# Performance work log

Hardware: AMD Instinct MI355X
Metric: run time of the kernel (lower is better)

## Reference

```python
import jax, jax.numpy as jnp
import numpy as np

INPUT_SZ, HIDDEN_SZ, OUTPUT_SZ, NUM_LAYERS, EMBED_SZ = 128, 512, 64, 4, 16
SEQ_LEN, BATCH = 128, 256


def setup_inputs() -> dict:
    key = jax.random.key(0)
    ks = jax.random.split(key, 12)
    H, E, L = HIDDEN_SZ, EMBED_SZ, NUM_LAYERS
    s = 0.05
    inp = {
        "input": jax.random.randint(ks[0], (SEQ_LEN, BATCH), 0, INPUT_SZ),
        "embed": jax.random.normal(ks[1], (INPUT_SZ, E), jnp.float32) * s,
        # layer 0 (input dim = E), dims: [dir=2, 4H, in]
        "Wih0": jax.random.normal(ks[2], (2, 4 * H, E), jnp.float32) * s,
        "Whh0": jax.random.normal(ks[3], (2, 4 * H, H), jnp.float32) * s,
        "bih0": jax.random.normal(ks[4], (2, 4 * H), jnp.float32) * s,
        "bhh0": jax.random.normal(ks[5], (2, 4 * H), jnp.float32) * s,
        # layers 1..L-1 (input dim = 2H)
        "Wih": jax.random.normal(ks[6], (L - 1, 2, 4 * H, 2 * H), jnp.float32) * s,
        "Whh": jax.random.normal(ks[7], (L - 1, 2, 4 * H, H), jnp.float32) * s,
        "bih": jax.random.normal(ks[8], (L - 1, 2, 4 * H), jnp.float32) * s,
        "bhh": jax.random.normal(ks[9], (L - 1, 2, 4 * H), jnp.float32) * s,
        "fc_w": jax.random.normal(ks[10], (OUTPUT_SZ, 4 * L * H), jnp.float32) * s,
        "fc_b": jax.random.normal(ks[11], (OUTPUT_SZ,), jnp.float32) * s,
    }
    return inp


def _lstm_forward(tokens, embed, Wih0, Whh0, bih0, bhh0, Wih, Whh, bih, bhh, fc_w, fc_b):
    L, H = NUM_LAYERS, HIDDEN_SZ
    T, B = tokens.shape
    xs = embed[tokens]  # [T, B, E]

    def step(carry, x_t):
        h, c = carry  # each [L, 2, B, H]
        x = x_t       # [B, in_dim]
        new_h, new_c = [], []
        for l in range(L):
            Wi = Wih0 if l == 0 else Wih[l - 1]
            Wh = Whh0 if l == 0 else Whh[l - 1]
            b = (bih0 + bhh0) if l == 0 else (bih[l - 1] + bhh[l - 1])
            # both directions see the same single-timestep input (PyTorch
            # bidirectional LSTM called with seq_len=1 per step)
            gates = (jnp.einsum('bi,dgi->dbg', x, Wi)
                     + jnp.einsum('dbh,dgh->dbg', h[l], Wh)
                     + b[:, None, :])  # [2, B, 4H]
            i_g, f_g, g_g, o_g = jnp.split(gates, 4, axis=-1)
            c_new = jax.nn.sigmoid(f_g) * c[l] + jax.nn.sigmoid(i_g) * jnp.tanh(g_g)
            h_new = jax.nn.sigmoid(o_g) * jnp.tanh(c_new)  # [2, B, H]
            new_h.append(h_new)
            new_c.append(c_new)
            x = jnp.concatenate([h_new[0], h_new[1]], axis=-1)  # [B, 2H]
        return (jnp.stack(new_h), jnp.stack(new_c)), None

    h0 = jnp.zeros((L, 2, B, H), xs.dtype)
    c0 = jnp.zeros((L, 2, B, H), xs.dtype)
    (h, c), _ = jax.lax.scan(step, (h0, c0), xs)

    # PyTorch layout: [2L, B, H], layer-major / direction-minor
    h = h.reshape(2 * L, B, H)
    c = c.reshape(2 * L, B, H)
    hid = jnp.concatenate([h, c], axis=2)                 # [2L, B, 2H]
    hid = hid.transpose(1, 0, 2).reshape(B, 4 * L * H)    # cat over 2L slices on dim 1
    out = hid @ fc_w.T + fc_b
    # dropout is identity at inference
    return jax.nn.softmax(out, axis=1)


def reference(input, embed, Wih0, Whh0, bih0, bhh0, Wih, Whh, bih, bhh, fc_w, fc_b):
    return _lstm_forward(input, embed, Wih0, Whh0, bih0, bhh0, Wih, Whh, bih, bhh, fc_w, fc_b)
```

## Files before the change

kernel.cpp:

```cpp
#include <hip/hip_runtime.h>

using short8 = __attribute__((ext_vector_type(8))) short;
using f32x4  = __attribute__((ext_vector_type(4))) float;
using f32x2  = __attribute__((ext_vector_type(2))) float;

static constexpr size_t N_WF0 = (size_t)2*32*8*3*4*512;
static constexpr size_t N_WF1 = (size_t)6*32*8*6*4*512;
static constexpr size_t N_WF  = N_WF0 + N_WF1;
static constexpr size_t N_BSE = (size_t)8*2048;
static constexpr size_t N_XPE = (size_t)128*2*256*8;
static constexpr size_t N_HBE = (size_t)2*8*64*256*8;
static constexpr size_t N_CBE = (size_t)8*256*512;
static constexpr size_t N_FCT = (size_t)8192*64;
static constexpr size_t N_FL  = (size_t)8*128;

static constexpr size_t OFF_WF = 0;
static constexpr size_t OFF_BS = OFF_WF + N_WF*2;
static constexpr size_t OFF_XP = OFF_BS + N_BSE*4;
static constexpr size_t OFF_HB = OFF_XP + N_XPE*2;
static constexpr size_t OFF_CB = OFF_HB + N_HBE*2;
static constexpr size_t OFF_HF = OFF_CB + N_CBE*4;
static constexpr size_t OFF_FC = OFF_HF + N_CBE*4;
static constexpr size_t OFF_FL = OFF_FC + N_FCT*4;
static constexpr size_t WS_NEEDED = OFF_FL + N_FL*4;

__device__ __forceinline__ short f2bf(float f) {
  unsigned u = __float_as_uint(f);
  u += 0x7fff + ((u >> 16) & 1);
  return (short)(u >> 16);
}

__device__ __forceinline__ void wait_ge(int* f, int target) {
  while (__hip_atomic_load(f, __ATOMIC_RELAXED, __HIP_MEMORY_SCOPE_AGENT) < target)
    __builtin_amdgcn_s_sleep(2);
}

__global__ void k_prep_wf(const float* __restrict__ Wih0, const float* __restrict__ Whh0,
                          const float* __restrict__ Wih,  const float* __restrict__ Whh,
                          short* __restrict__ Wf) {
  size_t idx = (size_t)blockIdx.x * blockDim.x + threadIdx.x;
  if (idx >= N_WF) return;
  int j  = (int)(idx & 7);
  int lane = (int)((idx >> 3) & 63);
  int gt = (int)((idx >> 9) & 3);
  int lr = lane & 15, qq = lane >> 4;
  float v;
  if (idx < N_WF0) {
    size_t rest = idx >> 11;
    int sl = (int)(rest % 3); size_t r2 = rest / 3;
    int wvv = (int)(r2 & 7);  size_t r3 = r2 >> 3;
    int ncc = (int)(r3 & 31); int dd = (int)(r3 >> 5);
    int g = gt*512 + ncc*16 + lr;
    int k = (wvv*3 + sl)*32 + qq*8 + j;
    if (k < 16)       v = Wih0[((size_t)dd*2048 + g)*16 + k];
    else if (k < 64)  v = 0.f;
    else if (k < 576) v = Whh0[((size_t)dd*2048 + g)*512 + (k - 64)];
    else              v = 0.f;
  } else {
    size_t u = idx - N_WF0;
    size_t rest = u >> 11;
    int sl = (int)(rest % 6); size_t r2 = rest / 6;
    int wvv = (int)(r2 & 7);  size_t r3 = r2 >> 3;
    int ncc = (int)(r3 & 31); int ldm = (int)(r3 >> 5);
    int g = gt*512 + ncc*16 + lr;
    int k = (wvv*6 + sl)*32 + qq*8 + j;
    if (k < 1024) v = Wih[((size_t)ldm*2048 + g)*1024 + k];
    else          v = Whh[((size_t)ldm*2048 + g)*512 + (k - 1024)];
  }
  Wf[idx] = f2bf(v);
}

__global__ void k_prep_bias(const float* __restrict__ bih0, const float* __restrict__ bhh0,
                            const float* __restrict__ bih, const float* __restrict__ bhh,
                            float* __restrict__ bsum) {
  int idx = blockIdx.x * blockDim.x + threadIdx.x;
  if (idx >= (int)N_BSE) return;
  int g = idx & 2047;
  int dd = (idx >> 11) & 1;
  int ll = idx >> 12;
  float v;
  if (ll == 0) v = bih0[dd*2048 + g] + bhh0[dd*2048 + g];
  else         v = bih[((ll-1)*2 + dd)*2048 + g] + bhh[((ll-1)*2 + dd)*2048 + g];
  bsum[idx] = v;
}

__global__ void k_prep_xp(const int* __restrict__ tok, const float* __restrict__ embed,
                          short* __restrict__ XP) {
  int idx = blockIdx.x * blockDim.x + threadIdx.x;
  if (idx >= (int)N_XPE) return;
  int i  = idx & 7;
  int b  = (idx >> 3) & 255;
  int kg = (idx >> 11) & 1;
  int t  = idx >> 12;
  int k = kg*8 + i;
  XP[idx] = f2bf(embed[tok[t*256 + b]*16 + k]);
}

__global__ void k_prep_fcT(const float* __restrict__ fc_w, float* __restrict__ fcT) {
  int idx = blockIdx.x * blockDim.x + threadIdx.x;
  if (idx >= (int)N_FCT) return;
  int o = idx & 63;
  int k = idx >> 6;
  fcT[idx] = fc_w[o * 8192 + k];
}

__global__ void __launch_bounds__(512, 2)
k_lstm(const short* __restrict__ Wf, const float* __restrict__ bsum,
       const short* __restrict__ XP, short* __restrict__ hb,
       float* __restrict__ cb, float* __restrict__ hf, int* __restrict__ Fl) {
  const int blk = blockIdx.x;
  const int ld = blk & 7, nc = blk >> 3;
  const int l = ld >> 1, d = ld & 1;
  const int tid = threadIdx.x;
  const int wv = tid >> 6, lane = tid & 63;
  const int q = lane >> 4, lr = lane & 15;
  const int SLb = (l == 0) ? 3 : 6;
  const size_t HB_LD = 131072;

  __shared__ float red[2][8][4][16][16];

  const int eu  = tid >> 7;
  const int en  = (tid >> 3) & 15;
  const int emh = tid & 7;
  float bias4[4];
  if (tid < 256) {
    #pragma unroll
    for (int gt = 0; gt < 4; ++gt)
      bias4[gt] = bsum[ld*2048 + gt*512 + nc*16 + en];
  }

  short8 wreg[6][4];
  {
    const short* wb = (l == 0)
      ? (Wf + (size_t)(d*32 + nc) * (8*3*4*512) + (size_t)wv * (3*4*512))
      : (Wf + N_WF0 + (size_t)((ld - 2)*32 + nc) * (8*6*4*512) + (size_t)wv * (6*4*512));
    #pragma unroll
    for (int sl = 0; sl < 6; ++sl) {
      #pragma unroll
      for (int gt = 0; gt < 4; ++gt) {
        if (sl < SLb) wreg[sl][gt] = *(const short8*)(wb + (sl*4 + gt)*512 + lane*8);
        else          wreg[sl][gt] = short8{0,0,0,0,0,0,0,0};
      }
    }
  }

  float* cbl = cb + (size_t)ld * (256*512);

  for (int t = 0; t < 128; ++t) {
    if (tid == 0) {
      if (t > 0) wait_ge(Fl + ld*128 + (t-1), 32);
      if (l > 0) {
        wait_ge(Fl + (ld-2-d)*128 + t, 32);
        wait_ge(Fl + (ld-1-d)*128 + t, 32);
      }
      if (l < 3 && t >= 2) {
        wait_ge(Fl + (2*l+2)*128 + (t-2), 32);
        wait_ge(Fl + (2*l+3)*128 + (t-2), 32);
      }
    }
    __syncthreads();
    __builtin_amdgcn_fence(__ATOMIC_ACQUIRE, "agent");

    const int pt = t & 1, pm = pt ^ 1;
    const short* apl[6];
    #pragma unroll
    for (int sl = 0; sl < 6; ++sl) {
      int S = wv * SLb + sl;
      const short* p; int lo;
      if (l == 0) {
        if (S < 2) { p = XP + (size_t)t * 4096; lo = (q < 1 ? q : 1) * 2048 + lr * 8; }
        else {
          int klb = (S <= 17) ? (4*S - 8) : 0;
          p = hb + (size_t)(pm*8 + ld) * HB_LD + (size_t)klb * 2048;
          lo = q * 2048 + lr * 8;
        }
      } else {
        const int pl0 = ld - 2 - d;
        if (S < 16)      p = hb + (size_t)(pt*8 + pl0    ) * HB_LD + (size_t)(4*S      ) * 2048;
        else if (S < 32) p = hb + (size_t)(pt*8 + pl0 + 1) * HB_LD + (size_t)(4*S - 64 ) * 2048;
        else             p = hb + (size_t)(pm*8 + ld     ) * HB_LD + (size_t)(4*S - 128) * 2048;
        lo = q * 2048 + lr * 8;
      }
      apl[sl] = p + lo;
    }

    short8 a[6][2];
    #pragma unroll
    for (int sl = 0; sl < 6; ++sl)
      if (sl < SLb) {
        a[sl][0] = *(const short8*)(apl[sl]);
        a[sl][1] = *(const short8*)(apl[sl] + 128);
      }

    for (int ro = 0; ro < 8; ++ro) {
      float c0 = 0.f, c1 = 0.f; int b0 = 0, b1 = 0, ej = 0;
      if (tid < 256) {
        ej = nc*16 + en;
        b0 = (ro*2 + eu)*16 + emh*2;
        b1 = b0 + 1;
        c0 = cbl[(size_t)b0*512 + ej];
        c1 = cbl[(size_t)b1*512 + ej];
      }
      f32x4 acc[2][4];
      #pragma unroll
      for (int u = 0; u < 2; ++u)
        #pragma unroll
        for (int gt = 0; gt < 4; ++gt) acc[u][gt] = f32x4{0.f,0.f,0.f,0.f};
      #pragma unroll
      for (int sl = 0; sl < 6; ++sl)
        if (sl < SLb) {
          #pragma unroll
          for (int gt = 0; gt < 4; ++gt) {
            acc[0][gt] = __builtin_amdgcn_mfma_f32_16x16x32_bf16(a[sl][0], wreg[sl][gt], acc[0][gt], 0,0,0);
            acc[1][gt] = __builtin_amdgcn_mfma_f32_16x16x32_bf16(a[sl][1], wreg[sl][gt], acc[1][gt], 0,0,0);
          }
        }
      if (ro < 7) {
        const int mo = (ro + 1) * 256;
        #pragma unroll
        for (int sl = 0; sl < 6; ++sl)
          if (sl < SLb) {
            a[sl][0] = *(const short8*)(apl[sl] + mo);
            a[sl][1] = *(const short8*)(apl[sl] + mo + 128);
          }
      }
      #pragma unroll
      for (int u = 0; u < 2; ++u)
        #pragma unroll
        for (int gt = 0; gt < 4; ++gt)
          *(f32x4*)&red[u][wv][gt][lr][q*4] = acc[u][gt];
      __syncthreads();
      if (tid < 256) {
        float g2[4][2];
        #pragma unroll
        for (int gt = 0; gt < 4; ++gt) {
          f32x2 sum = f32x2{0.f, 0.f};
          #pragma unroll
          for (int w8 = 0; w8 < 8; ++w8)
            sum += *(const f32x2*)&red[eu][w8][gt][en][emh*2];
          g2[gt][0] = sum[0] + bias4[gt];
          g2[gt][1] = sum[1] + bias4[gt];
        }
        short* hw = hb + (size_t)(pt*8 + ld) * HB_LD;
        #pragma unroll
        for (int e = 0; e < 2; ++e) {
          float gi = g2[0][e], gf = g2[1][e], gg = g2[2][e], go = g2[3][e];
          float si = 1.f/(1.f + __expf(-gi));
          float sf = 1.f/(1.f + __expf(-gf));
          float so = 1.f/(1.f + __expf(-go));
          float tg = 1.f - 2.f/(1.f + __expf(2.f*gg));
          float cold = e ? c1 : c0;
          int   b    = e ? b1 : b0;
          float cn = sf * cold + si * tg;
          float tc = 1.f - 2.f/(1.f + __expf(2.f*cn));
          float hn = so * tc;
          cbl[(size_t)b*512 + ej] = cn;
          hw[((size_t)(ej >> 3) * 256 + b) * 8 + (ej & 7)] = f2bf(hn);
          if (t == 127) hf[((size_t)ld*256 + b)*512 + ej] = hn;
        }
      }
      __syncthreads();
    }

    if (tid == 0)
      __hip_atomic_fetch_add(Fl + ld*128 + t, 1, __ATOMIC_RELEASE, __HIP_MEMORY_SCOPE_AGENT);
  }
}

__global__ void __launch_bounds__(256)
k_fc(const float* __restrict__ hf, const float* __restrict__ cb,
     const float* __restrict__ fcT, const float* __restrict__ fc_b,
     float* __restrict__ out) {
  const int tid = threadIdx.x;
  const int o = tid & 63;
  const int qw = tid >> 6;
  const int bi = blockIdx.x * 4 + qw;
  __shared__ float hidc[4][128];
  float acc = 0.f;
  for (int k0 = 0; k0 < 8192; k0 += 128) {
    #pragma unroll
    for (int c = 0; c < 2; ++c) {
      int idx = tid + c * 256;
      int r = idx >> 7, kk = idx & 127;
      int k = k0 + kk;
      int sS = k >> 10, rem = k & 1023, part = rem >> 9, j = rem & 511;
      const float* src = part ? cb : hf;
      hidc[r][kk] = src[((size_t)sS * 256 + (blockIdx.x * 4 + r)) * 512 + j];
    }
    __syncthreads();
    const float* hrow = hidc[qw];
    #pragma unroll 8
    for (int kk = 0; kk < 128; ++kk)
      acc += hrow[kk] * fcT[(size_t)(k0 + kk) * 64 + o];
    __syncthreads();
  }
  float v = acc + fc_b[o];
  float m = v;
  #pragma unroll
  for (int off = 32; off; off >>= 1) m = fmaxf(m, __shfl_xor(m, off, 64));
  float e = __expf(v - m);
  float ssum = e;
  #pragma unroll
  for (int off = 32; off; off >>= 1) ssum += __shfl_xor(ssum, off, 64);
  out[bi * 64 + o] = e / ssum;
}

extern "C" void kernel_launch(void* const* d_in, const int* in_sizes, int n_in,
                              void* d_out, int out_size, void* d_ws, size_t ws_size,
                              hipStream_t stream) {
  const int*   tok   = (const int*)d_in[0];
  const float* embed = (const float*)d_in[1];
  const float* Wih0  = (const float*)d_in[2];
  const float* Whh0  = (const float*)d_in[3];
  const float* bih0  = (const float*)d_in[4];
  const float* bhh0  = (const float*)d_in[5];
  const float* Wih   = (const float*)d_in[6];
  const float* Whh   = (const float*)d_in[7];
  const float* bih   = (const float*)d_in[8];
  const float* bhh   = (const float*)d_in[9];
  const float* fc_w  = (const float*)d_in[10];
  const float* fc_b  = (const float*)d_in[11];
  float* out = (float*)d_out;

  if (ws_size < WS_NEEDED) return;

  char* ws = (char*)d_ws;
  short* Wfb  = (short*)(ws + OFF_WF);
  float* bsum = (float*)(ws + OFF_BS);
  short* XP   = (short*)(ws + OFF_XP);
  short* hbuf = (short*)(ws + OFF_HB);
  float* cbuf = (float*)(ws + OFF_CB);
  float* hfb  = (float*)(ws + OFF_HF);
  float* fcT  = (float*)(ws + OFF_FC);
  int*   flg  = (int*)  (ws + OFF_FL);

  hipMemsetAsync(ws + OFF_HB + N_HBE, 0, N_HBE, stream);
  hipMemsetAsync(ws + OFF_CB, 0, N_CBE * 4, stream);
  hipMemsetAsync(ws + OFF_FL, 0, N_FL * 4, stream);

  k_prep_wf  <<<(int)((N_WF  + 255) / 256), 256, 0, stream>>>(Wih0, Whh0, Wih, Whh, Wfb);
  k_prep_bias<<<(int)((N_BSE + 255) / 256), 256, 0, stream>>>(bih0, bhh0, bih, bhh, bsum);
  k_prep_xp  <<<(int)((N_XPE + 255) / 256), 256, 0, stream>>>(tok, embed, XP);
  k_prep_fcT <<<(int)((N_FCT + 255) / 256), 256, 0, stream>>>(fc_w, fcT);

  void* kargs[] = {(void*)&Wfb, (void*)&bsum, (void*)&XP,
                   (void*)&hbuf, (void*)&cbuf, (void*)&hfb, (void*)&flg};
  hipLaunchCooperativeKernel((void*)k_lstm, dim3(256), dim3(512), kargs, 0, stream);

  k_fc<<<64, 256, 0, stream>>>(hfb, cbuf, fcT, fc_b, out);
}
```

Measured before the change: 6.139 ms.

## Stream LSTM activations into LDS via async global_load_lds double buffering, keep cell state in LDS

```diff
diff --git a/kernel.cpp b/kernel.cpp
--- a/kernel.cpp
+++ b/kernel.cpp
@@ -2,7 +2,6 @@
 
 using short8 = __attribute__((ext_vector_type(8))) short;
 using f32x4  = __attribute__((ext_vector_type(4))) float;
-using f32x2  = __attribute__((ext_vector_type(2))) float;
 
 static constexpr size_t N_WF0 = (size_t)2*32*8*3*4*512;
 static constexpr size_t N_WF1 = (size_t)6*32*8*6*4*512;
@@ -24,6 +23,11 @@
 static constexpr size_t OFF_FL = OFF_FC + N_FCT*4;
 static constexpr size_t WS_NEEDED = OFF_FL + N_FL*4;
 
+static constexpr int LDS_A   = 2*8*6*1024;
+static constexpr int LDS_RED = 8*4*16*20*4;
+static constexpr int LDS_C   = 16*256*4;
+static constexpr int LDS_TOT = LDS_A + LDS_RED + LDS_C;
+
 __device__ __forceinline__ short f2bf(float f) {
   unsigned u = __float_as_uint(f);
   u += 0x7fff + ((u >> 16) & 1);
@@ -32,7 +36,19 @@
 
 __device__ __forceinline__ void wait_ge(int* f, int target) {
   while (__hip_atomic_load(f, __ATOMIC_RELAXED, __HIP_MEMORY_SCOPE_AGENT) < target)
-    __builtin_amdgcn_s_sleep(2);
+    __builtin_amdgcn_s_sleep(1);
+}
+
+__device__ __forceinline__ void dma16(const void* g, void* l) {
+  __builtin_amdgcn_global_load_lds((const __attribute__((address_space(1))) unsigned int*)g,
+                                   (__attribute__((address_space(3))) unsigned int*)l, 16, 0, 0);
+}
+
+__device__ __forceinline__ void lds_barrier() {
+  __builtin_amdgcn_sched_barrier(0);
+  __builtin_amdgcn_s_waitcnt(0xC07F);
+  __builtin_amdgcn_s_barrier();
+  __builtin_amdgcn_sched_barrier(0);
 }
 
 __global__ void k_prep_wf(const float* __restrict__ Wih0, const float* __restrict__ Whh0,
@@ -107,26 +123,32 @@
 __global__ void __launch_bounds__(512, 2)
 k_lstm(const short* __restrict__ Wf, const float* __restrict__ bsum,
        const short* __restrict__ XP, short* __restrict__ hb,
-       float* __restrict__ cb, float* __restrict__ hf, int* __restrict__ Fl) {
+       float* __restrict__ cF, float* __restrict__ hf, int* __restrict__ Fl) {
+  extern __shared__ char smem[];
+  char*  As  = smem;
+  float* red = (float*)(smem + LDS_A);
+  float* cL  = (float*)(smem + LDS_A + LDS_RED);
+
   const int blk = blockIdx.x;
   const int ld = blk & 7, nc = blk >> 3;
   const int l = ld >> 1, d = ld & 1;
   const int tid = threadIdx.x;
   const int wv = tid >> 6, lane = tid & 63;
   const int q = lane >> 4, lr = lane & 15;
-  const int SLb = (l == 0) ? 3 : 6;
+  const int li = lane & 15, lk = lane >> 4;
+  const int SL = (l == 0) ? 3 : 6;
+  const int SUMW = (l == 0) ? 6 : 8;
+  const bool act = (l > 0) || (wv < 6);
   const size_t HB_LD = 131072;
 
-  __shared__ float red[2][8][4][16][16];
-
-  const int eu  = tid >> 7;
-  const int en  = (tid >> 3) & 15;
-  const int emh = tid & 7;
-  float bias4[4];
+  for (int i = tid; i < 4096; i += 512) cL[i] = 0.f;
+
+  float b4[4];
   if (tid < 256) {
+    int en = tid & 15;
     #pragma unroll
     for (int gt = 0; gt < 4; ++gt)
-      bias4[gt] = bsum[ld*2048 + gt*512 + nc*16 + en];
+      b4[gt] = bsum[ld*2048 + gt*512 + nc*16 + en];
   }
 
   short8 wreg[6][4];
@@ -138,128 +160,113 @@
     for (int sl = 0; sl < 6; ++sl) {
       #pragma unroll
       for (int gt = 0; gt < 4; ++gt) {
-        if (sl < SLb) wreg[sl][gt] = *(const short8*)(wb + (sl*4 + gt)*512 + lane*8);
-        else          wreg[sl][gt] = short8{0,0,0,0,0,0,0,0};
-      }
-    }
-  }
-
-  float* cbl = cb + (size_t)ld * (256*512);
+        if (sl < SL) wreg[sl][gt] = *(const short8*)(wb + (sl*4 + gt)*512 + lane*8);
+        else         wreg[sl][gt] = short8{0,0,0,0,0,0,0,0};
+      }
+    }
+  }
+  __syncthreads();
 
   for (int t = 0; t < 128; ++t) {
-    if (tid == 0) {
-      if (t > 0) wait_ge(Fl + ld*128 + (t-1), 32);
-      if (l > 0) {
-        wait_ge(Fl + (ld-2-d)*128 + t, 32);
-        wait_ge(Fl + (ld-1-d)*128 + t, 32);
-      }
-      if (l < 3 && t >= 2) {
-        wait_ge(Fl + (2*l+2)*128 + (t-2), 32);
-        wait_ge(Fl + (2*l+3)*128 + (t-2), 32);
-      }
-    }
+    if (tid == 0 && t > 0)           wait_ge(Fl + ld*128 + (t-1), 32);
+    if (tid == 1 && l > 0)           wait_ge(Fl + (ld-2-d)*128 + t, 32);
+    if (tid == 2 && l > 0)           wait_ge(Fl + (ld-1-d)*128 + t, 32);
+    if (tid == 3 && l < 3 && t >= 2) wait_ge(Fl + (2*l+2)*128 + (t-2), 32);
+    if (tid == 4 && l < 3 && t >= 2) wait_ge(Fl + (2*l+3)*128 + (t-2), 32);
     __syncthreads();
     __builtin_amdgcn_fence(__ATOMIC_ACQUIRE, "agent");
 
     const int pt = t & 1, pm = pt ^ 1;
+
     const short* apl[6];
     #pragma unroll
     for (int sl = 0; sl < 6; ++sl) {
-      int S = wv * SLb + sl;
-      const short* p; int lo;
-      if (l == 0) {
-        if (S < 2) { p = XP + (size_t)t * 4096; lo = (q < 1 ? q : 1) * 2048 + lr * 8; }
-        else {
-          int klb = (S <= 17) ? (4*S - 8) : 0;
-          p = hb + (size_t)(pm*8 + ld) * HB_LD + (size_t)klb * 2048;
-          lo = q * 2048 + lr * 8;
+      if (sl < SL && act) {
+        int S = wv * SL + sl;
+        const short* p;
+        if (l == 0) {
+          if (S < 2) p = XP + (size_t)t*4096 + (size_t)(lk & 1)*2048;
+          else       p = hb + (size_t)(pm*8 + ld)*HB_LD + (size_t)(4*S - 8 + lk)*2048;
+        } else {
+          const int pl0 = ld - 2 - d;
+          if (S < 16)      p = hb + (size_t)(pt*8 + pl0    )*HB_LD + (size_t)(4*S       + lk)*2048;
+          else if (S < 32) p = hb + (size_t)(pt*8 + pl0 + 1)*HB_LD + (size_t)(4*S - 64  + lk)*2048;
+          else             p = hb + (size_t)(pm*8 + ld     )*HB_LD + (size_t)(4*S - 128 + lk)*2048;
         }
-      } else {
-        const int pl0 = ld - 2 - d;
-        if (S < 16)      p = hb + (size_t)(pt*8 + pl0    ) * HB_LD + (size_t)(4*S      ) * 2048;
-        else if (S < 32) p = hb + (size_t)(pt*8 + pl0 + 1) * HB_LD + (size_t)(4*S - 64 ) * 2048;
-        else             p = hb + (size_t)(pm*8 + ld     ) * HB_LD + (size_t)(4*S - 128) * 2048;
-        lo = q * 2048 + lr * 8;
-      }
-      apl[sl] = p + lo;
-    }
-
-    short8 a[6][2];
-    #pragma unroll
-    for (int sl = 0; sl < 6; ++sl)
-      if (sl < SLb) {
-        a[sl][0] = *(const short8*)(apl[sl]);
-        a[sl][1] = *(const short8*)(apl[sl] + 128);
-      }
-
-    for (int ro = 0; ro < 8; ++ro) {
-      float c0 = 0.f, c1 = 0.f; int b0 = 0, b1 = 0, ej = 0;
-      if (tid < 256) {
-        ej = nc*16 + en;
-        b0 = (ro*2 + eu)*16 + emh*2;
-        b1 = b0 + 1;
-        c0 = cbl[(size_t)b0*512 + ej];
-        c1 = cbl[(size_t)b1*512 + ej];
-      }
-      f32x4 acc[2][4];
-      #pragma unroll
-      for (int u = 0; u < 2; ++u)
-        #pragma unroll
-        for (int gt = 0; gt < 4; ++gt) acc[u][gt] = f32x4{0.f,0.f,0.f,0.f};
+        apl[sl] = p + li*8;
+      } else apl[sl] = nullptr;
+    }
+
+    if (act) {
       #pragma unroll
       for (int sl = 0; sl < 6; ++sl)
-        if (sl < SLb) {
-          #pragma unroll
-          for (int gt = 0; gt < 4; ++gt) {
-            acc[0][gt] = __builtin_amdgcn_mfma_f32_16x16x32_bf16(a[sl][0], wreg[sl][gt], acc[0][gt], 0,0,0);
-            acc[1][gt] = __builtin_amdgcn_mfma_f32_16x16x32_bf16(a[sl][1], wreg[sl][gt], acc[1][gt], 0,0,0);
+        if (sl < SL) dma16(apl[sl], As + ((0*8 + wv)*6 + sl)*1024);
+    }
+
+    for (int ro = 0; ro < 16; ++ro) {
+      if (act && ro < 15) {
+        #pragma unroll
+        for (int sl = 0; sl < 6; ++sl)
+          if (sl < SL) dma16(apl[sl] + (ro+1)*128, As + ((((ro+1)&1)*8 + wv)*6 + sl)*1024);
+      }
+      __builtin_amdgcn_sched_barrier(0);
+      if (act) {
+        if (ro < 15) { if (l == 0) __builtin_amdgcn_s_waitcnt(0xF73);
+                       else        __builtin_amdgcn_s_waitcnt(0xF76); }
+        else         __builtin_amdgcn_s_waitcnt(0xF70);
+      }
+      __builtin_amdgcn_sched_barrier(0);
+
+      if (act) {
+        const char* ab = As + (size_t)(((ro&1)*8 + wv)*6)*1024 + (size_t)lane*16;
+        f32x4 acc[4];
+        #pragma unroll
+        for (int gt = 0; gt < 4; ++gt) acc[gt] = f32x4{0.f,0.f,0.f,0.f};
+        #pragma unroll
+        for (int sl = 0; sl < 6; ++sl)
+          if (sl < SL) {
+            short8 af = *(const short8*)(ab + sl*1024);
+            #pragma unroll
+            for (int gt = 0; gt < 4; ++gt)
+              acc[gt] = __builtin_amdgcn_mfma_f32_16x16x32_bf16(af, wreg[sl][gt], acc[gt], 0,0,0);
           }
+        #pragma unroll
+        for (int gt = 0; gt < 4; ++gt)
+          *(f32x4*)&red[(((wv*4 + gt)*16) + lr)*20 + q*4] = acc[gt];
+      }
+      lds_barrier();
+
+      if (tid < 256) {
+        const int m  = tid >> 4;
+        const int en = tid & 15;
+        const int j  = nc*16 + en;
+        const int b  = ro*16 + m;
+        float g4[4];
+        #pragma unroll
+        for (int gt = 0; gt < 4; ++gt) {
+          float s = 0.f;
+          for (int w = 0; w < SUMW; ++w)
+            s += red[((w*4 + gt)*16 + en)*20 + m];
+          g4[gt] = s + b4[gt];
         }
-      if (ro < 7) {
-        const int mo = (ro + 1) * 256;
-        #pragma unroll
-        for (int sl = 0; sl < 6; ++sl)
-          if (sl < SLb) {
-            a[sl][0] = *(const short8*)(apl[sl] + mo);
-            a[sl][1] = *(const short8*)(apl[sl] + mo + 128);
-          }
-      }
-      #pragma unroll
-      for (int u = 0; u < 2; ++u)
-        #pragma unroll
-        for (int gt = 0; gt < 4; ++gt)
-          *(f32x4*)&red[u][wv][gt][lr][q*4] = acc[u][gt];
-      __syncthreads();
-      if (tid < 256) {
-        float g2[4][2];
-        #pragma unroll
-        for (int gt = 0; gt < 4; ++gt) {
-          f32x2 sum = f32x2{0.f, 0.f};
-          #pragma unroll
-          for (int w8 = 0; w8 < 8; ++w8)
-            sum += *(const f32x2*)&red[eu][w8][gt][en][emh*2];
-          g2[gt][0] = sum[0] + bias4[gt];
-          g2[gt][1] = sum[1] + bias4[gt];
+        float cold = cL[ro*256 + tid];
+        float si = 1.f/(1.f + __expf(-g4[0]));
+        float sf = 1.f/(1.f + __expf(-g4[1]));
+        float so = 1.f/(1.f + __expf(-g4[3]));
+        float tg = 1.f - 2.f/(1.f + __expf(2.f*g4[2]));
+        float cn = sf * cold + si * tg;
+        float tc = 1.f - 2.f/(1.f + __expf(2.f*cn));
+        float hn = so * tc;
+        cL[ro*256 + tid] = cn;
+        short* hw = hb + (size_t)(pt*8 + ld)*HB_LD;
+        hw[((size_t)(j >> 3)*256 + b)*8 + (j & 7)] = f2bf(hn);
+        if (t == 127) {
+          hf[((size_t)ld*256 + b)*512 + j] = hn;
+          cF[((size_t)ld*256 + b)*512 + j] = cn;
         }
-        short* hw = hb + (size_t)(pt*8 + ld) * HB_LD;
-        #pragma unroll
-        for (int e = 0; e < 2; ++e) {
-          float gi = g2[0][e], gf = g2[1][e], gg = g2[2][e], go = g2[3][e];
-          float si = 1.f/(1.f + __expf(-gi));
-          float sf = 1.f/(1.f + __expf(-gf));
-          float so = 1.f/(1.f + __expf(-go));
-          float tg = 1.f - 2.f/(1.f + __expf(2.f*gg));
-          float cold = e ? c1 : c0;
-          int   b    = e ? b1 : b0;
-          float cn = sf * cold + si * tg;
-          float tc = 1.f - 2.f/(1.f + __expf(2.f*cn));
-          float hn = so * tc;
-          cbl[(size_t)b*512 + ej] = cn;
-          hw[((size_t)(ej >> 3) * 256 + b) * 8 + (ej & 7)] = f2bf(hn);
-          if (t == 127) hf[((size_t)ld*256 + b)*512 + ej] = hn;
-        }
-      }
-      __syncthreads();
+      }
+      if (ro < 15) lds_barrier();
+      else         __syncthreads();
     }
 
     if (tid == 0)
@@ -329,13 +336,12 @@
   float* bsum = (float*)(ws + OFF_BS);
   short* XP   = (short*)(ws + OFF_XP);
   short* hbuf = (short*)(ws + OFF_HB);
-  float* cbuf = (float*)(ws + OFF_CB);
+  float* cFb  = (float*)(ws + OFF_CB);
   float* hfb  = (float*)(ws + OFF_HF);
   float* fcT  = (float*)(ws + OFF_FC);
   int*   flg  = (int*)  (ws + OFF_FL);
 
   hipMemsetAsync(ws + OFF_HB + N_HBE, 0, N_HBE, stream);
-  hipMemsetAsync(ws + OFF_CB, 0, N_CBE * 4, stream);
   hipMemsetAsync(ws + OFF_FL, 0, N_FL * 4, stream);
 
   k_prep_wf  <<<(int)((N_WF  + 255) / 256), 256, 0, stream>>>(Wih0, Whh0, Wih, Whh, Wfb);
@@ -343,9 +349,14 @@
   k_prep_xp  <<<(int)((N_XPE + 255) / 256), 256, 0, stream>>>(tok, embed, XP);
   k_prep_fcT <<<(int)((N_FCT + 255) / 256), 256, 0, stream>>>(fc_w, fcT);
 
+  static bool attr_set = false;
+  (void)hipFuncSetAttribute((const void*)k_lstm,
+                            hipFuncAttributeMaxDynamicSharedMemorySize, LDS_TOT);
+  (void)attr_set;
+
   void* kargs[] = {(void*)&Wfb, (void*)&bsum, (void*)&XP,
-                   (void*)&hbuf, (void*)&cbuf, (void*)&hfb, (void*)&flg};
-  hipLaunchCooperativeKernel((void*)k_lstm, dim3(256), dim3(512), kargs, 0, stream);
-
-  k_fc<<<64, 256, 0, stream>>>(hfb, cbuf, fcT, fc_b, out);
-}
+                   (void*)&hbuf, (void*)&cFb, (void*)&hfb, (void*)&flg};
+  hipLaunchCooperativeKernel((void*)k_lstm, dim3(256), dim3(512), kargs, LDS_TOT, stream);
+
+  k_fc<<<64, 256, 0, stream>>>(hfb, cFb, fcT, fc_b, out);
+}
```

Measured after the change: 7.812 ms. +27.2%, slower.
